# Optimization experiments

Measured on AMD Instinct MI355X. Metric: run time of the kernel, lower is better.

## Reference

```python
import jax, jax.numpy as jnp
import numpy as np

S = 2048        # seq_len (number of rigid bodies)
D = 256         # node_dim
H = 16          # num_heads
C = 64          # num_channels
SPATIAL_DIM = 3
QUATERNION_DIM = 4


def setup_inputs() -> dict:
    key = jax.random.key(0)
    ks = jax.random.split(key, 9)
    nodes = jax.random.normal(ks[0], (S, D), jnp.float32)
    pos = jax.random.normal(ks[1], (S, 2 * SPATIAL_DIM), jnp.float32)
    rot = jax.random.normal(ks[2], (S, QUATERNION_DIM), jnp.float32)
    w = 0.02
    Wn = jax.random.normal(ks[3], (2 * H * C, D), jnp.float32) * w
    bn = jnp.zeros((2 * H * C,), jnp.float32)
    Wp = jax.random.normal(ks[4], (2 * H * C, 2 * SPATIAL_DIM), jnp.float32) * w
    bp = jnp.zeros((2 * H * C,), jnp.float32)
    Wr = jax.random.normal(ks[5], (2 * H * C, QUATERNION_DIM), jnp.float32) * w  # no bias
    Wv = jax.random.normal(ks[6], (3 * H * D, D), jnp.float32) * w
    bv = jnp.zeros((3 * H * D,), jnp.float32)
    return {"nodes": nodes, "pos": pos, "rot": rot,
            "Wn": Wn, "bn": bn, "Wp": Wp, "bp": bp, "Wr": Wr,
            "Wv": Wv, "bv": bv}


def _kq(x, W, b):
    # eqx.nn.Linear: y = W @ x + b, vmapped over seq -> x @ W.T + b
    y = x @ W.T
    if b is not None:
        y = y + b
    y = y.reshape(x.shape[0], H, 2 * C)
    k, q = jnp.split(y, 2, axis=-1)  # each (S, H, C)
    return k, q


def reference(nodes, pos, rot, Wn, bn, Wp, bp, Wr, Wv, bv):
    seq_len = nodes.shape[0]
    nodes_k, nodes_q = _kq(nodes, Wn, bn)
    pos_k, pos_q = _kq(pos, Wp, bp)
    rot_k, rot_q = _kq(rot, Wr, None)
    k = jnp.concatenate([nodes_k, pos_k, rot_k], axis=-2)  # (S, 3H, C)
    q = jnp.concatenate([nodes_q, pos_q, rot_q], axis=-2)  # (S, 3H, C)
    val = (nodes @ Wv.T + bv).reshape(seq_len, 3 * H, D)   # (S, 3H, D)
    logits = jnp.einsum('ihc,jhc->ijh', k, q)              # (S, S, 3H)
    # square the rotation-source logits (last H of the 3H head axis)
    logits = logits.at[..., -H:].set(jnp.square(logits[..., -H:]))
    logits = logits / jnp.sqrt(jnp.float32(H))
    att = jax.nn.softmax(logits, axis=-2)                  # softmax over key axis j
    out = jnp.einsum('ijh,jhd->id', att, val)              # (S, D)
    return out
```

## Files before the change

### kernel.cpp

```cpp
#include <hip/hip_runtime.h>
#include <hip/hip_bf16.h>

typedef __bf16 bf16;
typedef __attribute__((ext_vector_type(8)))  __bf16 bf16x8;
typedef __attribute__((ext_vector_type(4)))  __bf16 bf16x4;
typedef __attribute__((ext_vector_type(4)))  float  f32x4;

#define SEQ   2048
#define NDIM  256
#define NH3   48
#define CH    64
#define SQS   72
#define SVS   72
#define SPS   72
#define VTS   2176

#define OFF_NODES 0
#define OFF_POS   524288
#define OFF_ROT   536576
#define OFF_WN    544768
#define OFF_BN    1069056
#define OFF_WP    1071104
#define OFF_BP    1083392
#define OFF_WR    1085440
#define OFF_WV    1093632
#define OFF_BV    4239360
#define TOT_IN    4251648

__device__ bf16  g_in[TOT_IN];
__device__ bf16  g_k [NH3 * SEQ * CH];
__device__ bf16  g_q [NH3 * SEQ * CH];
__device__ bf16  g_vt[NH3 * NDIM * VTS];
__device__ float g_part[(size_t)NH3 * SEQ * NDIM];
__device__ int   g_isf32;

__global__ __launch_bounds__(256) void detect_k(const unsigned short* __restrict__ p) {
    __shared__ int cff, czero;
    if (threadIdx.x == 0) { cff = 0; czero = 0; }
    __syncthreads();
    int ff = 0, zz = 0;
    for (int r = 0; r < 64; ++r) {
        int idx = threadIdx.x * 64 + r;
        unsigned short u = p[idx];
        if (((u >> 7) & 0xFF) == 0xFF) ff++;
        if (((idx & 1) == 0) && (u == 0)) zz++;
    }
    if (ff) atomicAdd(&cff, ff);
    if (zz) atomicAdd(&czero, zz);
    __syncthreads();
    if (threadIdx.x == 0) g_isf32 = (cff > 2 || czero > 6000) ? 1 : 0;
}

__global__ __launch_bounds__(256) void convert_k(
    const void* s0, const void* s1, const void* s2, const void* s3, const void* s4,
    const void* s5, const void* s6, const void* s7, const void* s8, const void* s9)
{
    const void* srcs[10] = {s0, s1, s2, s3, s4, s5, s6, s7, s8, s9};
    const int   szs[10]  = {524288, 12288, 8192, 524288, 2048, 12288, 2048, 8192, 3145728, 12288};
    const int   offs[10] = {OFF_NODES, OFF_POS, OFF_ROT, OFF_WN, OFF_BN,
                            OFF_WP, OFF_BP, OFF_WR, OFF_WV, OFF_BV};
    const int y = blockIdx.y;
    const void* src = srcs[y];
    bf16* dst = g_in + offs[y];
    const int n = szs[y];
    const int isf = g_isf32;
    const int stride = gridDim.x * 256 * 4;
    for (int i = (blockIdx.x * 256 + threadIdx.x) * 4; i < n; i += stride) {
        bf16x4 o;
        if (isf) {
            float4 v = *(const float4*)((const float*)src + i);
            o[0] = (bf16)v.x; o[1] = (bf16)v.y; o[2] = (bf16)v.z; o[3] = (bf16)v.w;
        } else {
            o = *(const bf16x4*)((const bf16*)src + i);
        }
        *(bf16x4*)(dst + i) = o;
    }
}

__global__ __launch_bounds__(256) void proj_nodes_kq()
{
    __shared__ __align__(16) bf16 sB[64 * 264];
    const bf16* nodes = g_in + OFF_NODES;
    const bf16* Wn    = g_in + OFF_WN;
    const bf16* bn    = g_in + OFF_BN;
    const int t  = threadIdx.x;
    const int s0 = blockIdx.x * 64;
    const int f0 = blockIdx.y * 64;

    for (int rep = 0; rep < 8; ++rep) {
        int idx = t + rep * 256;
        int row = idx >> 5, chunk = idx & 31;
        *(bf16x8*)&sB[row * 264 + chunk * 8] =
            *(const bf16x8*)&Wn[(f0 + row) * 256 + chunk * 8];
    }
    __syncthreads();

    const int w = t >> 6, lane = t & 63;
    const int l15 = lane & 15, quad = lane >> 4;

    f32x4 acc[4] = {{}, {}, {}, {}};
    const bf16* arow = nodes + (s0 + w * 16 + l15) * 256 + quad * 8;
#pragma unroll
    for (int kc = 0; kc < 8; ++kc) {
        bf16x8 af = *(const bf16x8*)(arow + kc * 32);
#pragma unroll
        for (int ft = 0; ft < 4; ++ft) {
            bf16x8 bfr = *(const bf16x8*)&sB[(ft * 16 + l15) * 264 + kc * 32 + quad * 8];
            acc[ft] = __builtin_amdgcn_mfma_f32_16x16x32_bf16(af, bfr, acc[ft], 0, 0, 0);
        }
    }
#pragma unroll
    for (int ft = 0; ft < 4; ++ft) {
        int f = f0 + ft * 16 + l15;
        float bias = (float)bn[f];
        int h = f >> 7, c2 = f & 127;
        bf16* base = (c2 < 64) ? (g_k + h * SEQ * CH + c2)
                               : (g_q + h * SEQ * CH + (c2 - 64));
#pragma unroll
        for (int r = 0; r < 4; ++r) {
            int s = s0 + w * 16 + quad * 4 + r;
            base[s * CH] = (bf16)(acc[ft][r] + bias);
        }
    }
}

__global__ __launch_bounds__(256) void proj_posrot_kq()
{
    const bf16* pos  = g_in + OFF_POS;
    const bf16* rotq = g_in + OFF_ROT;
    const bf16* Wp   = g_in + OFF_WP;
    const bf16* bp   = g_in + OFF_BP;
    const bf16* Wr   = g_in + OFF_WR;
    int id = blockIdx.x * 256 + threadIdx.x;
    int fg  = id & 511;
    int s   = (id >> 9) & 2047;
    int src = id >> 20;
    int f0  = fg * 4;
    float y[4]; int h;
    if (src == 0) {
#pragma unroll
        for (int j = 0; j < 4; ++j) {
            float a = (float)bp[f0 + j];
#pragma unroll
            for (int x = 0; x < 6; ++x)
                a += (float)pos[s * 6 + x] * (float)Wp[(f0 + j) * 6 + x];
            y[j] = a;
        }
        h = 16 + (f0 >> 7);
    } else {
#pragma unroll
        for (int j = 0; j < 4; ++j) {
            float a = 0.f;
#pragma unroll
            for (int x = 0; x < 4; ++x)
                a += (float)rotq[s * 4 + x] * (float)Wr[(f0 + j) * 4 + x];
            y[j] = a;
        }
        h = 32 + (f0 >> 7);
    }
    bf16x4 o;
#pragma unroll
    for (int j = 0; j < 4; ++j) o[j] = (bf16)y[j];
    int c2 = f0 & 127;
    if (c2 < 64) *(bf16x4*)&g_k[(h * SEQ + s) * CH + c2]        = o;
    else         *(bf16x4*)&g_q[(h * SEQ + s) * CH + (c2 - 64)] = o;
}

__global__ __launch_bounds__(256) void proj_v()
{
    __shared__ __align__(16) bf16 sB[64 * 264];
    __shared__ __align__(16) bf16 sO[64 * 72];
    const bf16* nodes = g_in + OFF_NODES;
    const bf16* Wv    = g_in + OFF_WV;
    const bf16* bv    = g_in + OFF_BV;
    const int t  = threadIdx.x;
    const int s0 = blockIdx.x * 64;
    const int f0 = blockIdx.y * 64;

    for (int rep = 0; rep < 8; ++rep) {
        int idx = t + rep * 256;
        int row = idx >> 5, chunk = idx & 31;
        *(bf16x8*)&sB[row * 264 + chunk * 8] =
            *(const bf16x8*)&Wv[(f0 + row) * 256 + chunk * 8];
    }
    __syncthreads();

    const int w = t >> 6, lane = t & 63;
    const int l15 = lane & 15, quad = lane >> 4;

    f32x4 acc[4] = {{}, {}, {}, {}};
    const bf16* arow = nodes + (s0 + w * 16 + l15) * 256 + quad * 8;
#pragma unroll
    for (int kc = 0; kc < 8; ++kc) {
        bf16x8 af = *(const bf16x8*)(arow + kc * 32);
#pragma unroll
        for (int ft = 0; ft < 4; ++ft) {
            bf16x8 bfr = *(const bf16x8*)&sB[(ft * 16 + l15) * 264 + kc * 32 + quad * 8];
            acc[ft] = __builtin_amdgcn_mfma_f32_16x16x32_bf16(af, bfr, acc[ft], 0, 0, 0);
        }
    }
    __syncthreads();
#pragma unroll
    for (int ft = 0; ft < 4; ++ft) {
        int n = f0 + ft * 16 + l15;
        float bias = (float)bv[n];
#pragma unroll
        for (int r = 0; r < 4; ++r) {
            sO[(ft * 16 + l15) * 72 + (quad * 4 + r) * 4 + w] = (bf16)(acc[ft][r] + bias);
        }
    }
    __syncthreads();
    for (int rep = 0; rep < 2; ++rep) {
        int idx = t + rep * 256;
        int row = idx >> 3, chunk = idx & 7;
        *(bf16x8*)&g_vt[(size_t)(f0 + row) * VTS + s0 + chunk * 8] =
            *(const bf16x8*)&sO[row * 72 + chunk * 8];
    }
}

__global__ __launch_bounds__(512, 4) void attn_k()
{
    const int bx  = blockIdx.x;
    const int xcd = bx & 7;
    const int sub = bx >> 3;
    const int h   = xcd * 6 + (sub % 6);
    const int it  = sub / 6;
    const int i0  = it * 128;
    const int t   = threadIdx.x;
    const int w   = t >> 6, lane = t & 63;
    const int l15 = lane & 15, quad = lane >> 4;
    const bool rot = (h >= 32);

    __shared__ __align__(16) bf16 sQ[64 * SQS];
    __shared__ __align__(16) bf16 sV[256 * SVS];
    __shared__ __align__(16) bf16 sP[128 * SPS];
    __shared__ float sL[128];

    const bf16* kb = g_k  + h * SEQ * CH;
    const bf16* qb = g_q  + h * SEQ * CH;
    const bf16* vb = g_vt + (size_t)h * NDIM * VTS;

    bf16x8 kf0 = *(const bf16x8*)&kb[(i0 + w * 16 + l15) * CH + quad * 8];
    bf16x8 kf1 = *(const bf16x8*)&kb[(i0 + w * 16 + l15) * CH + 32 + quad * 8];

    const int ih = w >> 2, dq = w & 3;

    f32x4 acc[4][4];
#pragma unroll
    for (int a = 0; a < 4; ++a)
#pragma unroll
        for (int b = 0; b < 4; ++b) acc[a][b] = (f32x4){0.f, 0.f, 0.f, 0.f};
    f32x4 lp = {0.f, 0.f, 0.f, 0.f};

    for (int st = 0; st < 32; ++st) {
        {
            int row = t >> 3, ch = t & 7;
            *(bf16x8*)&sQ[row * SQS + ch * 8] = *(const bf16x8*)&qb[st * 4096 + t * 8];
#pragma unroll
            for (int rep = 0; rep < 4; ++rep) {
                int idx = t + rep * 512;
                int vr = idx >> 3, vc = idx & 7;
                *(bf16x8*)&sV[vr * SVS + vc * 8] =
                    *(const bf16x8*)&vb[(size_t)vr * VTS + st * 64 + vc * 8];
            }
        }
        __syncthreads();

        f32x4 sjb[4];
#pragma unroll
        for (int jb = 0; jb < 4; ++jb) {
            bf16x8 q0 = *(const bf16x8*)&sQ[(jb * 16 + l15) * SQS + quad * 8];
            bf16x8 q1 = *(const bf16x8*)&sQ[(jb * 16 + l15) * SQS + 32 + quad * 8];
            f32x4 sa = {};
            sa = __builtin_amdgcn_mfma_f32_16x16x32_bf16(kf0, q0, sa, 0, 0, 0);
            sa = __builtin_amdgcn_mfma_f32_16x16x32_bf16(kf1, q1, sa, 0, 0, 0);
            sjb[jb] = sa;
        }

#pragma unroll
        for (int r = 0; r < 4; ++r) {
            bf16x4 pk;
#pragma unroll
            for (int jb = 0; jb < 4; ++jb) {
                float d = sjb[jb][r];
                float x = rot ? (d * d * 0.25f) : (d * 0.25f);
                x = fminf(x, 60.f);
                float p = __expf(x);
                lp[r] += p;
                pk[jb] = (bf16)p;
            }
            *(bf16x4*)&sP[(w * 16 + quad * 4 + r) * SPS + l15 * 4] = pk;
        }
        __syncthreads();

#pragma unroll
        for (int kc = 0; kc < 2; ++kc) {
            bf16x8 ap[4], vf[4];
#pragma unroll
            for (int itr = 0; itr < 4; ++itr)
                ap[itr] = *(const bf16x8*)&sP[(ih * 64 + itr * 16 + l15) * SPS + kc * 32 + quad * 8];
#pragma unroll
            for (int dt = 0; dt < 4; ++dt)
                vf[dt] = *(const bf16x8*)&sV[(dq * 64 + dt * 16 + l15) * SVS + kc * 32 + quad * 8];
#pragma unroll
            for (int itr = 0; itr < 4; ++itr)
#pragma unroll
                for (int dt = 0; dt < 4; ++dt)
                    acc[itr][dt] = __builtin_amdgcn_mfma_f32_16x16x32_bf16(
                        ap[itr], vf[dt], acc[itr][dt], 0, 0, 0);
        }
        __syncthreads();
    }

#pragma unroll
    for (int off = 1; off < 16; off <<= 1) {
#pragma unroll
        for (int r = 0; r < 4; ++r) lp[r] += __shfl_xor(lp[r], off, 64);
    }
    if (l15 == 0) *(f32x4*)&sL[w * 16 + quad * 4] = lp;
    __syncthreads();

    float* pb = g_part + (size_t)h * SEQ * NDIM;
#pragma unroll
    for (int itr = 0; itr < 4; ++itr) {
        f32x4 lv = *(const f32x4*)&sL[ih * 64 + itr * 16 + quad * 4];
#pragma unroll
        for (int r = 0; r < 4; ++r) {
            float inv = 1.0f / lv[r];
            float* ob = &pb[(size_t)(i0 + ih * 64 + itr * 16 + quad * 4 + r) * NDIM + dq * 64 + l15];
#pragma unroll
            for (int dt = 0; dt < 4; ++dt)
                ob[dt * 16] = acc[itr][dt][r] * inv;
        }
    }
}

__global__ __launch_bounds__(256) void finalize_k(float* __restrict__ out) {
    int idx = (blockIdx.x * 256 + threadIdx.x) * 4;
    f32x4 s = {0.f, 0.f, 0.f, 0.f};
#pragma unroll
    for (int hh = 0; hh < NH3; ++hh)
        s += *(const f32x4*)&g_part[(size_t)hh * SEQ * NDIM + idx];
    *(f32x4*)&out[idx] = s;
}

extern "C" void kernel_launch(void* const* d_in, const int* in_sizes, int n_in,
                              void* d_out, int out_size, void* d_ws, size_t ws_size,
                              hipStream_t stream) {
    detect_k <<<dim3(1),        dim3(256), 0, stream>>>((const unsigned short*)d_in[8]);
    convert_k<<<dim3(768, 10),  dim3(256), 0, stream>>>(d_in[0], d_in[1], d_in[2], d_in[3],
                                                        d_in[4], d_in[5], d_in[6], d_in[7],
                                                        d_in[8], d_in[9]);
    proj_nodes_kq <<<dim3(32, 32),  dim3(256), 0, stream>>>();
    proj_posrot_kq<<<dim3(8192),    dim3(256), 0, stream>>>();
    proj_v        <<<dim3(32, 192), dim3(256), 0, stream>>>();
    attn_k        <<<dim3(768),     dim3(512), 0, stream>>>();
    finalize_k    <<<dim3(512),     dim3(256), 0, stream>>>((float*)d_out);
}
```

Before: 384.9 us.

## Prefetch next Q/V tile into registers in attention; XCD-aware block remap for projections

```diff
diff --git a/kernel.cpp b/kernel.cpp
--- a/kernel.cpp
+++ b/kernel.cpp
@@ -83,9 +83,12 @@
     const bf16* nodes = g_in + OFF_NODES;
     const bf16* Wn    = g_in + OFF_WN;
     const bf16* bn    = g_in + OFF_BN;
-    const int t  = threadIdx.x;
-    const int s0 = blockIdx.x * 64;
-    const int f0 = blockIdx.y * 64;
+    const int t    = threadIdx.x;
+    const int bx   = blockIdx.x;
+    const int xcd  = bx & 7;
+    const int rest = bx >> 3;
+    const int f0   = (xcd * 4 + (rest & 3)) * 64;
+    const int s0   = (rest >> 2) * 64;
 
     for (int rep = 0; rep < 8; ++rep) {
         int idx = t + rep * 256;
@@ -173,15 +176,18 @@
     const bf16* nodes = g_in + OFF_NODES;
     const bf16* Wv    = g_in + OFF_WV;
     const bf16* bv    = g_in + OFF_BV;
-    const int t  = threadIdx.x;
-    const int s0 = blockIdx.x * 64;
-    const int f0 = blockIdx.y * 64;
+    const int t    = threadIdx.x;
+    const int bx   = blockIdx.x;
+    const int xcd  = bx & 7;
+    const int rest = bx >> 3;
+    const int f0   = (xcd * 24 + (rest % 24)) * 64;
+    const int s0   = (rest / 24) * 64;
 
     for (int rep = 0; rep < 8; ++rep) {
         int idx = t + rep * 256;
         int row = idx >> 5, chunk = idx & 31;
         *(bf16x8*)&sB[row * 264 + chunk * 8] =
-            *(const bf16x8*)&Wv[(f0 + row) * 256 + chunk * 8];
+            *(const bf16x8*)&Wv[(size_t)(f0 + row) * 256 + chunk * 8];
     }
     __syncthreads();
 
@@ -245,6 +251,8 @@
 
     const int ih = w >> 2, dq = w & 3;
 
+    const int qrow = t >> 3, qch = t & 7;
+
     f32x4 acc[4][4];
 #pragma unroll
     for (int a = 0; a < 4; ++a)
@@ -252,20 +260,22 @@
         for (int b = 0; b < 4; ++b) acc[a][b] = (f32x4){0.f, 0.f, 0.f, 0.f};
     f32x4 lp = {0.f, 0.f, 0.f, 0.f};
 
+    bf16x8 qpre, vpre[4];
+    qpre = *(const bf16x8*)&qb[t * 8];
+#pragma unroll
+    for (int rep = 0; rep < 4; ++rep) {
+        int idx = t + rep * 512;
+        vpre[rep] = *(const bf16x8*)&vb[(size_t)(idx >> 3) * VTS + (idx & 7) * 8];
+    }
+    *(bf16x8*)&sQ[qrow * SQS + qch * 8] = qpre;
+#pragma unroll
+    for (int rep = 0; rep < 4; ++rep) {
+        int idx = t + rep * 512;
+        *(bf16x8*)&sV[(idx >> 3) * SVS + (idx & 7) * 8] = vpre[rep];
+    }
+    __syncthreads();
+
     for (int st = 0; st < 32; ++st) {
-        {
-            int row = t >> 3, ch = t & 7;
-            *(bf16x8*)&sQ[row * SQS + ch * 8] = *(const bf16x8*)&qb[st * 4096 + t * 8];
-#pragma unroll
-            for (int rep = 0; rep < 4; ++rep) {
-                int idx = t + rep * 512;
-                int vr = idx >> 3, vc = idx & 7;
-                *(bf16x8*)&sV[vr * SVS + vc * 8] =
-                    *(const bf16x8*)&vb[(size_t)vr * VTS + st * 64 + vc * 8];
-            }
-        }
-        __syncthreads();
-
         f32x4 sjb[4];
 #pragma unroll
         for (int jb = 0; jb < 4; ++jb) {
@@ -293,6 +303,17 @@
         }
         __syncthreads();
 
+        if (st < 31) {
+            const bf16* qn = qb + (st + 1) * 4096;
+            const bf16* vn = vb + (st + 1) * 64;
+            qpre = *(const bf16x8*)&qn[t * 8];
+#pragma unroll
+            for (int rep = 0; rep < 4; ++rep) {
+                int idx = t + rep * 512;
+                vpre[rep] = *(const bf16x8*)&vn[(size_t)(idx >> 3) * VTS + (idx & 7) * 8];
+            }
+        }
+
 #pragma unroll
         for (int kc = 0; kc < 2; ++kc) {
             bf16x8 ap[4], vf[4];
@@ -310,6 +331,16 @@
                         ap[itr], vf[dt], acc[itr][dt], 0, 0, 0);
         }
         __syncthreads();
+
+        if (st < 31) {
+            *(bf16x8*)&sQ[qrow * SQS + qch * 8] = qpre;
+#pragma unroll
+            for (int rep = 0; rep < 4; ++rep) {
+                int idx = t + rep * 512;
+                *(bf16x8*)&sV[(idx >> 3) * SVS + (idx & 7) * 8] = vpre[rep];
+            }
+            __syncthreads();
+        }
     }
 
 #pragma unroll
@@ -351,9 +382,9 @@
     convert_k<<<dim3(768, 10),  dim3(256), 0, stream>>>(d_in[0], d_in[1], d_in[2], d_in[3],
                                                         d_in[4], d_in[5], d_in[6], d_in[7],
                                                         d_in[8], d_in[9]);
-    proj_nodes_kq <<<dim3(32, 32),  dim3(256), 0, stream>>>();
-    proj_posrot_kq<<<dim3(8192),    dim3(256), 0, stream>>>();
-    proj_v        <<<dim3(32, 192), dim3(256), 0, stream>>>();
-    attn_k        <<<dim3(768),     dim3(512), 0, stream>>>();
-    finalize_k    <<<dim3(512),     dim3(256), 0, stream>>>((float*)d_out);
-}
+    proj_nodes_kq <<<dim3(1024),  dim3(256), 0, stream>>>();
+    proj_posrot_kq<<<dim3(8192),  dim3(256), 0, stream>>>();
+    proj_v        <<<dim3(6144),  dim3(256), 0, stream>>>();
+    attn_k        <<<dim3(768),   dim3(512), 0, stream>>>();
+    finalize_k    <<<dim3(512),   dim3(256), 0, stream>>>((float*)d_out);
+}
```

New measurement: 333.7 us. 13.3% less time.
